# Kernel optimization log

Hardware: AMD Instinct MI355X
Metric: run time of the kernel (lower is better)

Reference implementation:

```python
import jax, jax.numpy as jnp
import numpy as np

BS, FH, FW, NA = 32, 100, 100, 9
IMG_H, IMG_W = 1600, 1600
STRIDE = 16
KEEP_PRE, KEEP_POST, NMS_THR = 1000, 300, 0.7


def _grid_anchors():
    scales = np.array([128.0, 256.0, 512.0])
    ratios = np.array([0.5, 1.0, 2.0])
    ws, hs = [], []
    for s in scales:
        for r in ratios:
            ws.append(s * np.sqrt(1.0 / r))
            hs.append(s * np.sqrt(r))
    ws, hs = np.array(ws), np.array(hs)  # [9]
    sx = (np.arange(FW) + 0.5) * STRIDE
    sy = (np.arange(FH) + 0.5) * STRIDE
    cx, cy = np.meshgrid(sx, sy)  # [FH,FW]
    cx = cx.reshape(-1, 1)
    cy = cy.reshape(-1, 1)
    anchors = np.stack([
        cx - 0.5 * ws, cy - 0.5 * hs, cx + 0.5 * ws, cy + 0.5 * hs
    ], axis=-1).reshape(-1, 4)  # [FH*FW*NA, 4]
    return anchors.astype(np.float32)


def setup_inputs() -> dict:
    key = jax.random.key(0)
    k1, k2 = jax.random.split(key)
    N = FH * FW * NA
    cls_logits = jax.random.normal(k1, (BS, N, 1), dtype=jnp.float32)
    reg_deltas = jax.random.normal(k2, (BS, N, 4), dtype=jnp.float32) * 0.3
    anchors = jnp.asarray(_grid_anchors())
    return {"cls_logits": cls_logits, "reg_deltas": reg_deltas,
            "anchors": anchors, "img_h": IMG_H, "img_w": IMG_W}


def _offsets2boxes(deltas, anchors):
    # deltas: [bs,N,4] (dx,dy,dw,dh); anchors: [N,4] xyxy
    aw = anchors[:, 2] - anchors[:, 0]
    ah = anchors[:, 3] - anchors[:, 1]
    acx = anchors[:, 0] + 0.5 * aw
    acy = anchors[:, 1] + 0.5 * ah
    cx = deltas[..., 0] * aw + acx
    cy = deltas[..., 1] * ah + acy
    w = jnp.exp(deltas[..., 2]) * aw
    h = jnp.exp(deltas[..., 3]) * ah
    return jnp.stack([cx - 0.5 * w, cy - 0.5 * h, cx + 0.5 * w, cy + 0.5 * h], axis=-1)


def _iou_matrix(b):
    # b: [K,4] -> [K,K]
    area = (b[:, 2] - b[:, 0]) * (b[:, 3] - b[:, 1])
    lt = jnp.maximum(b[:, None, :2], b[None, :, :2])
    rb = jnp.minimum(b[:, None, 2:], b[None, :, 2:])
    wh = jnp.clip(rb - lt, 0.0)
    inter = wh[..., 0] * wh[..., 1]
    return inter / (area[:, None] + area[None, :] - inter + 1e-12)


def _detect_single(boxes, scores, img_h, img_w):
    # boxes: [N,4], scores: [N]
    top_scores, idx = jax.lax.top_k(scores, KEEP_PRE)
    b = boxes[idx]  # [K,4], already score-sorted descending
    b = jnp.stack([
        jnp.clip(b[:, 0], 0.0, img_w), jnp.clip(b[:, 1], 0.0, img_h),
        jnp.clip(b[:, 2], 0.0, img_w), jnp.clip(b[:, 3], 0.0, img_h)
    ], axis=-1)
    iou = _iou_matrix(b)  # [K,K]
    K = KEEP_PRE
    cols = jnp.arange(K)

    def body(i, keep):
        # if box i still kept, suppress later boxes with IoU > thr (greedy NMS)
        sup = keep[i] & (iou[i] > NMS_THR) & (cols > i)
        return keep & ~sup

    keep = jax.lax.fori_loop(0, K, body, jnp.ones((K,), dtype=bool))
    # kept boxes first (stable sort preserves descending-score order), take top P
    order = jnp.argsort(~keep, stable=True)[:KEEP_POST]
    valid = keep[order]
    det = jnp.concatenate([b[order], top_scores[order, None]], axis=-1)
    return det * valid[:, None].astype(det.dtype)  # padded rows zeroed


def reference(cls_logits, reg_deltas, anchors, img_h, img_w):
    bs = cls_logits.shape[0]
    scores = jax.nn.sigmoid(cls_logits.reshape(bs, -1))  # [bs,N]
    boxes = _offsets2boxes(reg_deltas.reshape(bs, -1, 4), anchors)  # [bs,N,4]
    fh = jnp.float32(img_h)
    fw = jnp.float32(img_w)
    dets = jax.vmap(lambda b, s: _detect_single(b, s, fh, fw))(boxes, scores)
    return dets  # [bs, KEEP_POST, 5] (xmin,ymin,xmax,ymax,score), zero-padded
```

## Files before the change

kernel.cpp:

```cpp
#include <hip/hip_runtime.h>
#include <stdint.h>

#pragma clang fp contract(off)

#define BS 32
#define NANCH 90000
#define KEEP_PRE 1000
#define KEEP_POST 300
#define NMS_THR 0.7f
#define NBINS 4096
#define HREP 4129
#define MW 16
#define NF4 22500
#define NSL 8
#define F4_PER_BLK ((NF4 + NSL - 1) / NSL)
#define SLICE_CAP 1536
#define MERGE_CAP 2048

typedef unsigned long long u64;
typedef unsigned int u32;

#define CNTG_OFF  0
#define CAND_OFF  1024
#define BOX_OFF   (CAND_OFF + (size_t)BS * NSL * SLICE_CAP * 8)
#define SCORE_OFF (BOX_OFF + (size_t)BS * KEEP_PRE * 16)
#define MASK_OFF  (SCORE_OFF + (size_t)BS * KEEP_PRE * 4)

__device__ __forceinline__ u32 fmono(float f) {
    u32 u = __float_as_uint(f);
    return (u & 0x80000000u) ? ~u : (u | 0x80000000u);
}

__global__ __launch_bounds__(1024) void sel_kernel(const float* __restrict__ logits,
                                                   u32* __restrict__ cntg,
                                                   u64* __restrict__ cand) {
    __shared__ u32 mono[F4_PER_BLK * 4 + 12];
    __shared__ u32 lh[2][HREP];
    __shared__ u32 wtot[16], wexc[16];
    __shared__ u32 s_B, s_cnt;
    const int b = blockIdx.y, slice = blockIdx.x, tid = threadIdx.x;
    const u32 lane = tid & 63;
    const int wv = tid >> 6;

    for (int i = tid; i < 2 * HREP; i += 1024) ((u32*)lh)[i] = 0;
    if (tid == 0) s_cnt = 0;
    __syncthreads();

    const float4* src4 = (const float4*)(logits + (size_t)b * NANCH);
    const int f0 = slice * F4_PER_BLK;
    const int f1 = min(f0 + F4_PER_BLK, NF4);
    const int nf = f1 - f0;
    u32* myh = lh[tid & 1];
    for (int j = tid; j < nf; j += 1024) {
        float4 v = src4[f0 + j];
        u32 m0 = fmono(v.x), m1 = fmono(v.y), m2 = fmono(v.z), m3 = fmono(v.w);
        *(uint4*)&mono[j * 4] = make_uint4(m0, m1, m2, m3);
        atomicAdd(&myh[m0 >> 20], 1u);
        atomicAdd(&myh[m1 >> 20], 1u);
        atomicAdd(&myh[m2 >> 20], 1u);
        atomicAdd(&myh[m3 >> 20], 1u);
    }
    __syncthreads();

    const int g = tid * 4;
    const u32 c0 = lh[0][g] + lh[1][g];
    const u32 c1 = lh[0][g + 1] + lh[1][g + 1];
    const u32 c2 = lh[0][g + 2] + lh[1][g + 2];
    const u32 c3 = lh[0][g + 3] + lh[1][g + 3];
    u32 sc = c0 + c1 + c2 + c3;
#pragma unroll
    for (int off = 1; off < 64; off <<= 1) {
        u32 x = __shfl_down(sc, off);
        if (lane + off < 64) sc += x;
    }
    if (lane == 0) wtot[wv] = sc;
    __syncthreads();
    if (tid < 16) {
        u32 v = wtot[tid];
        u32 t = v;
#pragma unroll
        for (int off = 1; off < 16; off <<= 1) {
            u32 x = __shfl_down(t, off);
            if (tid + off < 16) t += x;
        }
        wexc[tid] = t - v;
    }
    __syncthreads();
    {
        const u32 S0 = wexc[wv] + sc;
        const u32 S1 = S0 - c0, S2 = S1 - c1, S3 = S2 - c2, S4 = S3 - c3;
        if (S0 >= KEEP_PRE && S1 < KEEP_PRE) s_B = (u32)g;
        if (S1 >= KEEP_PRE && S2 < KEEP_PRE) s_B = (u32)(g + 1);
        if (S2 >= KEEP_PRE && S3 < KEEP_PRE) s_B = (u32)(g + 2);
        if (S3 >= KEEP_PRE && S4 < KEEP_PRE) s_B = (u32)(g + 3);
    }
    __syncthreads();
    const u32 B = s_B;

    const int ntot = nf * 4;
    const int npad = ((ntot + 1023) & ~1023);
    u64* dst = cand + ((size_t)b * NSL + slice) * SLICE_CAP;
    for (int i = tid; i < npad; i += 1024) {
        u32 m = (i < ntot) ? mono[i] : 0u;
        bool is = (i < ntot) && ((m >> 20) >= B);
        u64 bal = __ballot(is);
        if (bal) {
            u32 old = 0;
            if (lane == 0) old = atomicAdd(&s_cnt, (u32)__popcll(bal));
            u32 wbase = __shfl(old, 0);
            if (is) {
                u32 prefix = (u32)__popcll(bal & ((1ull << lane) - 1ull));
                u32 pos = wbase + prefix;
                if (pos < SLICE_CAP) {
                    u32 gi = (u32)(f0 * 4 + i);
                    dst[pos] = ((u64)m << 32) | (u32)(~gi);
                }
            }
        }
    }
    __syncthreads();
    if (tid == 0) cntg[b * NSL + slice] = min(s_cnt, (u32)SLICE_CAP);
}

__global__ __launch_bounds__(1024) void merge_kernel(const float* __restrict__ deltas,
                                                     const float* __restrict__ anchors,
                                                     const u32* __restrict__ cntg,
                                                     const u64* __restrict__ cand,
                                                     float4* __restrict__ selbox,
                                                     float* __restrict__ selscore,
                                                     const int* __restrict__ p_img_h,
                                                     const int* __restrict__ p_img_w) {
    __shared__ u32 lh[HREP];
    __shared__ u32 S[NBINS + 1];
    __shared__ u32 start[NBINS];
    __shared__ u64 grp[MERGE_CAP];
    __shared__ u32 wtot[16], wexc[16];
    __shared__ u32 s_B;
    const int b = blockIdx.x, tid = threadIdx.x;
    const u32 lane = tid & 63;
    const int wv = tid >> 6;

    for (int i = tid; i < HREP; i += 1024) lh[i] = 0;
    __syncthreads();

    u32 cnts[NSL];
#pragma unroll
    for (int k = 0; k < NSL; k++) cnts[k] = cntg[b * NSL + k];
    const u64* src = cand + (size_t)b * NSL * SLICE_CAP;

#pragma unroll
    for (int k = 0; k < NSL; k++) {
        const u64* ss = src + (size_t)k * SLICE_CAP;
        for (int i = tid; i < (int)cnts[k]; i += 1024)
            atomicAdd(&lh[(u32)(ss[i] >> 52)], 1u);
    }
    __syncthreads();

    const int g = tid * 4;
    const u32 c0 = lh[g], c1 = lh[g + 1], c2 = lh[g + 2], c3 = lh[g + 3];
    u32 sc = c0 + c1 + c2 + c3;
#pragma unroll
    for (int off = 1; off < 64; off <<= 1) {
        u32 x = __shfl_down(sc, off);
        if (lane + off < 64) sc += x;
    }
    if (lane == 0) wtot[wv] = sc;
    __syncthreads();
    if (tid < 16) {
        u32 v = wtot[tid];
        u32 t = v;
#pragma unroll
        for (int off = 1; off < 16; off <<= 1) {
            u32 x = __shfl_down(t, off);
            if (tid + off < 16) t += x;
        }
        wexc[tid] = t - v;
    }
    __syncthreads();
    {
        const u32 S0 = wexc[wv] + sc;
        const u32 S1 = S0 - c0, S2 = S1 - c1, S3 = S2 - c2, S4 = S3 - c3;
        S[g] = S0; S[g + 1] = S1; S[g + 2] = S2; S[g + 3] = S3;
        if (tid == 1023) S[NBINS] = 0;
        start[g] = S1; start[g + 1] = S2; start[g + 2] = S3; start[g + 3] = S4;
        if (S0 >= KEEP_PRE && S1 < KEEP_PRE) s_B = (u32)g;
        if (S1 >= KEEP_PRE && S2 < KEEP_PRE) s_B = (u32)(g + 1);
        if (S2 >= KEEP_PRE && S3 < KEEP_PRE) s_B = (u32)(g + 2);
        if (S3 >= KEEP_PRE && S4 < KEEP_PRE) s_B = (u32)(g + 3);
    }
    __syncthreads();
    const u32 B = s_B;
    const int n_cap = (int)min(S[B], (u32)MERGE_CAP);

#pragma unroll
    for (int k = 0; k < NSL; k++) {
        const u64* ss = src + (size_t)k * SLICE_CAP;
        for (int i = tid; i < (int)cnts[k]; i += 1024) {
            u64 key = ss[i];
            u32 bin = (u32)(key >> 52);
            if (bin >= B) {
                u32 pos = atomicAdd(&start[bin], 1u);
                if (pos < (u32)MERGE_CAP) grp[pos] = key;
            }
        }
    }
    __syncthreads();

    const float W = (float)(*p_img_w);
    const float H = (float)(*p_img_h);
    const float4* d4 = (const float4*)deltas;
    const float4* a4 = (const float4*)anchors;
    for (int p = tid; p < n_cap; p += 1024) {
        const u64 me = grp[p];
        const int bin = (int)(me >> 52);
        const int gb = (int)S[bin + 1];
        const int ge = min((int)S[bin], n_cap);
        int rank = gb;
        int q = gb;
        for (; q + 4 <= ge; q += 4) {
            rank += (grp[q] > me) + (grp[q + 1] > me)
                  + (grp[q + 2] > me) + (grp[q + 3] > me);
        }
        for (; q < ge; q++) rank += (grp[q] > me);
        if (rank < KEEP_PRE) {
            u32 idx = ~(u32)me;
            u32 m = (u32)(me >> 32);
            u32 ub = (m & 0x80000000u) ? (m ^ 0x80000000u) : ~m;
            float logit = __uint_as_float(ub);
            float score = 1.0f / (1.0f + expf(-logit));
            float4 d = d4[(size_t)b * NANCH + idx];
            float4 a = a4[idx];
            float aw = a.z - a.x, ah = a.w - a.y;
            float acx = a.x + 0.5f * aw, acy = a.y + 0.5f * ah;
            float cx = d.x * aw + acx, cy = d.y * ah + acy;
            float w = expf(d.z) * aw, h = expf(d.w) * ah;
            float x1 = cx - 0.5f * w, y1 = cy - 0.5f * h;
            float x2 = cx + 0.5f * w, y2 = cy + 0.5f * h;
            x1 = fminf(fmaxf(x1, 0.0f), W); y1 = fminf(fmaxf(y1, 0.0f), H);
            x2 = fminf(fmaxf(x2, 0.0f), W); y2 = fminf(fmaxf(y2, 0.0f), H);
            selbox[(size_t)b * KEEP_PRE + rank] = make_float4(x1, y1, x2, y2);
            selscore[(size_t)b * KEEP_PRE + rank] = score;
        }
    }
}

__global__ __launch_bounds__(256) void iou_kernel(const float4* __restrict__ selbox,
                                                  u64* __restrict__ mask) {
    const int b = blockIdx.y;
    const int bx = blockIdx.x;
    int c, w;
    if (bx < 16)      { c = 0; w = bx; }
    else if (bx < 28) { c = 1; w = bx - 12; }
    else if (bx < 36) { c = 2; w = bx - 20; }
    else              { c = 3; w = bx - 24; }
    const int i = c * 256 + threadIdx.x;
    __shared__ float4 cb[64];
    __shared__ float ca[64];
    if (threadIdx.x < 64) {
        int j = w * 64 + threadIdx.x;
        float4 bx4 = (j < KEEP_PRE) ? selbox[(size_t)b * KEEP_PRE + j]
                                    : make_float4(0, 0, 0, 0);
        cb[threadIdx.x] = bx4;
        ca[threadIdx.x] = (bx4.z - bx4.x) * (bx4.w - bx4.y);
    }
    __syncthreads();
    if (i >= KEEP_PRE) return;
    float4 bi = selbox[(size_t)b * KEEP_PRE + i];
    float ai = (bi.z - bi.x) * (bi.w - bi.y);
    const int jbase = w * 64;
    u64 bits = 0;
#pragma unroll 8
    for (int jj = 0; jj < 64; jj++) {
        float4 bj = cb[jj];
        float ltx = fmaxf(bi.x, bj.x), lty = fmaxf(bi.y, bj.y);
        float rbx = fminf(bi.z, bj.z), rby = fminf(bi.w, bj.w);
        float wx = fmaxf(rbx - ltx, 0.0f), wy = fmaxf(rby - lty, 0.0f);
        float inter = wx * wy;
        float denom = ai + ca[jj] - inter + 1e-12f;
        if (inter / denom > NMS_THR) bits |= (1ull << jj);
    }
    int lo = i + 1 - jbase;
    u64 mlo = (lo <= 0) ? ~0ull : ((lo >= 64) ? 0ull : (~0ull << lo));
    int hi = KEEP_PRE - jbase;
    u64 mhi = (hi >= 64) ? ~0ull : ((1ull << hi) - 1ull);
    mask[((size_t)b * KEEP_PRE + i) * MW + w] = bits & mlo & mhi;
}

#define CH_ROWS 64
#define CH_WORDS (CH_ROWS * MW)
#define NCHUNK ((KEEP_PRE + CH_ROWS - 1) / CH_ROWS)

__global__ __launch_bounds__(256) void nms_out_kernel(const u64* __restrict__ mask,
                                                      const float4* __restrict__ selbox,
                                                      const float* __restrict__ selscore,
                                                      float* __restrict__ out) {
    const int b = blockIdx.x;
    __shared__ u64 lbuf[2][CH_WORDS];
    __shared__ u64 keepw[MW];
    __shared__ u32 wpre[MW + 1];
    __shared__ int ls_stop;
    const int tid = threadIdx.x;
    const u64* mrow = mask + (size_t)b * KEEP_PRE * MW;

    auto load_chunk = [&](int c) {
        int idx = tid - 128;
        if (idx < 0) return;
        const int words = (c == NCHUNK - 1)
                            ? (KEEP_PRE - (NCHUNK - 1) * CH_ROWS) * MW
                            : CH_WORDS;
        const u64* gsrc = mrow + (size_t)c * CH_WORDS;
        u64* dst = lbuf[c & 1];
#pragma unroll
        for (int k = 0; k < 4; k++) {
            int off = k * 256 + idx * 2;
            ulonglong2 v;
            if (off < words) v = *(const ulonglong2*)(gsrc + off);
            else { v.x = 0ull; v.y = 0ull; }
            *(ulonglong2*)(dst + off) = v;
        }
    };

    if (tid == 0) ls_stop = 0;
    load_chunk(0);
    __syncthreads();

    u64 remv = 0;
    int kept_total = 0;
    const int lw = tid & 15;
    for (int c = 0; c < NCHUNK; c++) {
        if (c + 1 < NCHUNK) load_chunk(c + 1);
        if (tid < 64) {
            const u64* lb = lbuf[c & 1];
            const int wmin = (c >> 2) << 2;
            const u64 vmask = (lw >= wmin) ? ~0ull : 0ull;
            u64 cur = __shfl(remv, c);
#pragma unroll
            for (int blk = 0; blk < 8; blk++) {
                u64 R[8], rwv[8];
#pragma unroll
                for (int k = 0; k < 8; k++)
                    R[k] = lb[(size_t)(blk * 8 + k) * MW + lw] & vmask;
#pragma unroll
                for (int k = 0; k < 8; k++)
                    rwv[k] = lb[(size_t)(blk * 8 + k) * MW + c];
#pragma unroll
                for (int k = 0; k < 8; k++) {
                    const int p = blk * 8 + k;
                    u64 msk = ((cur >> p) & 1ull) ? 0ull : ~0ull;
                    remv |= R[k] & msk;
                    cur  |= rwv[k] & msk;
                }
            }
            kept_total += 64 - (int)__popcll(cur);
            if (c + 1 < NCHUNK && kept_total >= KEEP_POST) {
                if (lw > c) remv = ~0ull;
                if (tid == 0) ls_stop = 1;
            }
        }
        __syncthreads();
        if (ls_stop) break;
    }

    if (tid < MW) {
        u64 kw = ~remv;
        if (tid == MW - 1) kw &= (1ull << (KEEP_PRE - 64 * (MW - 1))) - 1ull;
        keepw[tid] = kw;
    }
    __syncthreads();
    if (tid == 0) {
        u32 cnt = 0;
        for (int w = 0; w < MW; w++) { wpre[w] = cnt; cnt += (u32)__popcll(keepw[w]); }
        wpre[MW] = cnt;
    }
    __syncthreads();
    const int total = (int)wpre[MW];
    float* outb = out + (size_t)b * KEEP_POST * 5;
    for (int i = tid; i < KEEP_PRE; i += 256) {
        int w = i >> 6;
        u64 kw = keepw[w];
        if ((kw >> (i & 63)) & 1ull) {
            int rank = (int)wpre[w] + __popcll(kw & ((1ull << (i & 63)) - 1ull));
            if (rank < KEEP_POST) {
                float4 bx = selbox[(size_t)b * KEEP_PRE + i];
                float sc = selscore[(size_t)b * KEEP_PRE + i];
                outb[rank * 5 + 0] = bx.x;
                outb[rank * 5 + 1] = bx.y;
                outb[rank * 5 + 2] = bx.z;
                outb[rank * 5 + 3] = bx.w;
                outb[rank * 5 + 4] = sc;
            }
        }
    }
    for (int r = tid; r < KEEP_POST; r += 256) {
        if (r >= total) {
            outb[r * 5 + 0] = 0.0f;
            outb[r * 5 + 1] = 0.0f;
            outb[r * 5 + 2] = 0.0f;
            outb[r * 5 + 3] = 0.0f;
            outb[r * 5 + 4] = 0.0f;
        }
    }
}

extern "C" void kernel_launch(void* const* d_in, const int* in_sizes, int n_in,
                              void* d_out, int out_size, void* d_ws, size_t ws_size,
                              hipStream_t stream) {
    const float* logits  = (const float*)d_in[0];
    const float* deltas  = (const float*)d_in[1];
    const float* anchors = (const float*)d_in[2];
    const int* p_img_h   = (const int*)d_in[3];
    const int* p_img_w   = (const int*)d_in[4];

    char* ws = (char*)d_ws;
    u32* cntg       = (u32*)(ws + CNTG_OFF);
    u64* cand       = (u64*)(ws + CAND_OFF);
    float4* selbox  = (float4*)(ws + BOX_OFF);
    float* selscore = (float*)(ws + SCORE_OFF);
    u64* mask       = (u64*)(ws + MASK_OFF);

    sel_kernel<<<dim3(NSL, BS), 1024, 0, stream>>>(logits, cntg, cand);
    merge_kernel<<<dim3(BS), 1024, 0, stream>>>(deltas, anchors, cntg, cand,
                                                selbox, selscore, p_img_h, p_img_w);
    iou_kernel<<<dim3(40, BS), 256, 0, stream>>>(selbox, mask);
    nms_out_kernel<<<BS, 256, 0, stream>>>(mask, selbox, selscore, (float*)d_out);
}
```

Baseline: 160.9 us.

## Drop LDS score staging, re-read logits, double slices and histogram copies

The selection kernel no longer stages the mono-converted logits in shared memory. It re-reads them from global memory, which should mostly hit cache, during the compaction pass. Cutting the LDS footprint lets the kernel use more slices per batch (16 instead of 8), four histogram copies to reduce atomic contention, and a higher occupancy hint. Costs are a second global read of the logits and more candidate slices for the merge kernel to combine.

```diff
diff --git a/kernel.cpp b/kernel.cpp
--- a/kernel.cpp
+++ b/kernel.cpp
@@ -10,9 +10,10 @@
 #define NMS_THR 0.7f
 #define NBINS 4096
 #define HREP 4129
+#define NCOPY 4
 #define MW 16
 #define NF4 22500
-#define NSL 8
+#define NSL 16
 #define F4_PER_BLK ((NF4 + NSL - 1) / NSL)
 #define SLICE_CAP 1536
 #define MERGE_CAP 2048
@@ -21,7 +22,7 @@
 typedef unsigned int u32;
 
 #define CNTG_OFF  0
-#define CAND_OFF  1024
+#define CAND_OFF  2048
 #define BOX_OFF   (CAND_OFF + (size_t)BS * NSL * SLICE_CAP * 8)
 #define SCORE_OFF (BOX_OFF + (size_t)BS * KEEP_PRE * 16)
 #define MASK_OFF  (SCORE_OFF + (size_t)BS * KEEP_PRE * 4)
@@ -31,18 +32,17 @@
     return (u & 0x80000000u) ? ~u : (u | 0x80000000u);
 }
 
-__global__ __launch_bounds__(1024) void sel_kernel(const float* __restrict__ logits,
-                                                   u32* __restrict__ cntg,
-                                                   u64* __restrict__ cand) {
-    __shared__ u32 mono[F4_PER_BLK * 4 + 12];
-    __shared__ u32 lh[2][HREP];
+__global__ __launch_bounds__(1024, 8) void sel_kernel(const float* __restrict__ logits,
+                                                      u32* __restrict__ cntg,
+                                                      u64* __restrict__ cand) {
+    __shared__ u32 lh[NCOPY][HREP];
     __shared__ u32 wtot[16], wexc[16];
     __shared__ u32 s_B, s_cnt;
     const int b = blockIdx.y, slice = blockIdx.x, tid = threadIdx.x;
     const u32 lane = tid & 63;
     const int wv = tid >> 6;
 
-    for (int i = tid; i < 2 * HREP; i += 1024) ((u32*)lh)[i] = 0;
+    for (int i = tid; i < NCOPY * HREP; i += 1024) ((u32*)lh)[i] = 0;
     if (tid == 0) s_cnt = 0;
     __syncthreads();
 
@@ -50,23 +50,21 @@
     const int f0 = slice * F4_PER_BLK;
     const int f1 = min(f0 + F4_PER_BLK, NF4);
     const int nf = f1 - f0;
-    u32* myh = lh[tid & 1];
+    u32* myh = lh[tid & (NCOPY - 1)];
     for (int j = tid; j < nf; j += 1024) {
         float4 v = src4[f0 + j];
-        u32 m0 = fmono(v.x), m1 = fmono(v.y), m2 = fmono(v.z), m3 = fmono(v.w);
-        *(uint4*)&mono[j * 4] = make_uint4(m0, m1, m2, m3);
-        atomicAdd(&myh[m0 >> 20], 1u);
-        atomicAdd(&myh[m1 >> 20], 1u);
-        atomicAdd(&myh[m2 >> 20], 1u);
-        atomicAdd(&myh[m3 >> 20], 1u);
+        atomicAdd(&myh[fmono(v.x) >> 20], 1u);
+        atomicAdd(&myh[fmono(v.y) >> 20], 1u);
+        atomicAdd(&myh[fmono(v.z) >> 20], 1u);
+        atomicAdd(&myh[fmono(v.w) >> 20], 1u);
     }
     __syncthreads();
 
     const int g = tid * 4;
-    const u32 c0 = lh[0][g] + lh[1][g];
-    const u32 c1 = lh[0][g + 1] + lh[1][g + 1];
-    const u32 c2 = lh[0][g + 2] + lh[1][g + 2];
-    const u32 c3 = lh[0][g + 3] + lh[1][g + 3];
+    const u32 c0 = lh[0][g] + lh[1][g] + lh[2][g] + lh[3][g];
+    const u32 c1 = lh[0][g + 1] + lh[1][g + 1] + lh[2][g + 1] + lh[3][g + 1];
+    const u32 c2 = lh[0][g + 2] + lh[1][g + 2] + lh[2][g + 2] + lh[3][g + 2];
+    const u32 c3 = lh[0][g + 3] + lh[1][g + 3] + lh[2][g + 3] + lh[3][g + 3];
     u32 sc = c0 + c1 + c2 + c3;
 #pragma unroll
     for (int off = 1; off < 64; off <<= 1) {
@@ -97,23 +95,29 @@
     __syncthreads();
     const u32 B = s_B;
 
-    const int ntot = nf * 4;
-    const int npad = ((ntot + 1023) & ~1023);
+    const int nfp = (nf + 1023) & ~1023;
     u64* dst = cand + ((size_t)b * NSL + slice) * SLICE_CAP;
-    for (int i = tid; i < npad; i += 1024) {
-        u32 m = (i < ntot) ? mono[i] : 0u;
-        bool is = (i < ntot) && ((m >> 20) >= B);
-        u64 bal = __ballot(is);
-        if (bal) {
-            u32 old = 0;
-            if (lane == 0) old = atomicAdd(&s_cnt, (u32)__popcll(bal));
-            u32 wbase = __shfl(old, 0);
-            if (is) {
-                u32 prefix = (u32)__popcll(bal & ((1ull << lane) - 1ull));
-                u32 pos = wbase + prefix;
-                if (pos < SLICE_CAP) {
-                    u32 gi = (u32)(f0 * 4 + i);
-                    dst[pos] = ((u64)m << 32) | (u32)(~gi);
+    for (int j = tid; j < nfp; j += 1024) {
+        const bool inb = j < nf;
+        float4 v = make_float4(0.f, 0.f, 0.f, 0.f);
+        if (inb) v = src4[f0 + j];
+        u32 mm[4];
+        mm[0] = fmono(v.x); mm[1] = fmono(v.y); mm[2] = fmono(v.z); mm[3] = fmono(v.w);
+#pragma unroll
+        for (int k = 0; k < 4; k++) {
+            bool is = inb && ((mm[k] >> 20) >= B);
+            u64 bal = __ballot(is);
+            if (bal) {
+                u32 old = 0;
+                if (lane == 0) old = atomicAdd(&s_cnt, (u32)__popcll(bal));
+                u32 wbase = __shfl(old, 0);
+                if (is) {
+                    u32 prefix = (u32)__popcll(bal & ((1ull << lane) - 1ull));
+                    u32 pos = wbase + prefix;
+                    if (pos < SLICE_CAP) {
+                        u32 gi = (u32)((f0 + j) * 4 + k);
+                        dst[pos] = ((u64)mm[k] << 32) | (u32)(~gi);
+                    }
                 }
             }
         }
```

Result: slower. 169.1 us (+5.1%).
